# Optimization experiments

Hardware: AMD Instinct MI355X
Metric: run time of the kernel (lower is better)

Reference implementation:

```python
import jax, jax.numpy as jnp
import numpy as np

NEAR, FAR = 0.05, 6.0
STEPSIZE = 0.5
ALPHA_INIT = 1e-6
XYZ_MIN = np.array([-1.0, -1.0, -1.0], np.float32)
XYZ_MAX = np.array([1.0, 1.0, 1.0], np.float32)
WORLD = (160, 160, 160)
VOXEL_SIZE = 2.0 / 160.0  # ((prod span)/num_voxels)^(1/3)
N_SAMPLES = int(np.linalg.norm(np.array(WORLD) + 1) / STEPSIZE) + 1  # 558
ACT_SHIFT = float(np.log(1.0 / (1.0 - ALPHA_INIT) - 1.0))


def setup_inputs() -> dict:
    key = jax.random.key(0)
    k1, k2, k3, k4, k5, k6, k7 = jax.random.split(key, 7)
    rays_o = (jax.random.uniform(k1, (8192, 3), jnp.float32) - 0.5) * 1.2  # inside bbox
    rd = jax.random.normal(k2, (8192, 3), jnp.float32)
    rays_d = rd / jnp.linalg.norm(rd, axis=-1, keepdims=True)
    jitter = jax.random.uniform(k3, (8192, 1), jnp.float32)
    em_modes = jax.random.randint(k4, (8192,), 0, 2, jnp.int32)
    density = jax.random.normal(k5, (1, 160, 160, 160), jnp.float32) * 0.1
    off_color = jax.random.normal(k6, (3, 160, 160, 160), jnp.float32) * 0.1
    emo_color = jax.random.normal(k7, (3, 160, 160, 160), jnp.float32) * 0.1
    return {"rays_o": rays_o, "rays_d": rays_d, "jitter": jitter, "em_modes": em_modes,
            "density": density, "off_color": off_color, "emo_color": emo_color}


def grid_sampler(pts, grid):
    """Trilinear interp, align_corners=True, zero padding. grid [C,Nx,Ny,Nz], pts [...,3] -> [...,C]."""
    C = grid.shape[0]
    sizes = np.array(grid.shape[1:], np.int32)
    lead = pts.shape[:-1]
    t = (pts.reshape(-1, 3) - XYZ_MIN) / (XYZ_MAX - XYZ_MIN)
    idx = t * (jnp.asarray(sizes, pts.dtype) - 1)  # voxel-space coords
    i0 = jnp.floor(idx).astype(jnp.int32)
    f = idx - i0.astype(pts.dtype)
    out = jnp.zeros((i0.shape[0], C), grid.dtype)
    for corner in range(8):
        off = np.array([(corner >> 2) & 1, (corner >> 1) & 1, corner & 1], np.int32)
        ci = i0 + off  # [N,3]
        w = jnp.prod(jnp.where(off[None, :] == 1, f, 1.0 - f), axis=-1)  # [N]
        valid = jnp.all((ci >= 0) & (ci < sizes[None, :]), axis=-1)
        cc = jnp.clip(ci, 0, sizes[None, :] - 1)
        vals = grid[:, cc[:, 0], cc[:, 1], cc[:, 2]].T  # [N,C]
        out = out + (w * valid)[:, None] * vals
    return out.reshape(*lead, C)


def sample_ray(rays_o, rays_d, jitter):
    vec = jnp.where(rays_d == 0, 1e-6, rays_d)
    rate_a = (XYZ_MAX - rays_o) / vec
    rate_b = (XYZ_MIN - rays_o) / vec
    t_min = jnp.clip(jnp.minimum(rate_a, rate_b).max(-1), NEAR, FAR)
    t_max = jnp.clip(jnp.maximum(rate_a, rate_b).min(-1), NEAR, FAR)
    mask_out = t_max <= t_min  # [R]
    rng = jnp.arange(N_SAMPLES, dtype=rays_o.dtype)[None, :] + jitter  # [R,S]
    step = STEPSIZE * VOXEL_SIZE * rng
    interpx = t_min[:, None] + step / jnp.linalg.norm(rays_d, axis=-1, keepdims=True)
    rays_pts = rays_o[:, None, :] + rays_d[:, None, :] * interpx[..., None]  # [R,S,3]
    mask_out = mask_out[:, None] | ((rays_pts < XYZ_MIN) | (rays_pts > XYZ_MAX)).any(-1)
    return rays_pts, mask_out


def reference(rays_o, rays_d, jitter, em_modes, density, off_color, emo_color):
    rays_pts, mask_out = sample_ray(rays_o, rays_d, jitter)
    dens = grid_sampler(rays_pts, density)[..., 0]  # [R,S]
    alpha_all = 1.0 - jnp.exp(-jax.nn.softplus(dens + ACT_SHIFT) * STEPSIZE)
    alpha = jnp.where(mask_out, 0.0, alpha_all)
    p = jnp.clip(1.0 - alpha, 1e-10, None)
    alphainv_cum = jnp.concatenate([jnp.ones_like(p[..., :1]), jnp.cumprod(p, -1)], -1)  # [R,S+1]
    weights = alpha * alphainv_cum[..., :-1]
    on_mask = (em_modes == 1)[:, None, None]
    emo = jax.nn.sigmoid(grid_sampler(rays_pts, emo_color))
    off = jax.nn.sigmoid(grid_sampler(rays_pts, off_color))
    rgb = jnp.where(on_mask, emo, 0.0) + off  # [R,S,3]
    rgb_marched = (weights[..., None] * rgb).sum(-2)  # [R,3]
    return (alphainv_cum, weights, alphainv_cum[..., -1:], rgb, rgb_marched)
```

## Files before the change

kernel.cpp:

```cpp
#include <hip/hip_runtime.h>
#include <math.h>


namespace {
constexpr int   kR   = 8192;
constexpr int   kS   = 558;
constexpr int   kG   = 160;
constexpr int   kG3  = kG * kG * kG;
constexpr float kNear = 0.05f;
constexpr float kFar  = 6.0f;
constexpr float kStepWorld = 0.5f * (2.0f / 160.0f);
constexpr float kActShift = -13.815509557963774f;
constexpr float kLog2e = 1.4426950408889634f;
constexpr int   kBX = 80, kBY = 80, kBZ = 40;
constexpr int   kNB = kBX * kBY * kBZ;
constexpr int   kGridWords = kNB * 16;
}

typedef unsigned int nuint4 __attribute__((ext_vector_type(4)));
typedef float        nfloat2 __attribute__((ext_vector_type(2)));
typedef float        nfloat4 __attribute__((ext_vector_type(4)));

__device__ __forceinline__ float fexp(float x) {
  return __builtin_amdgcn_exp2f(x * kLog2e);
}
__device__ __forceinline__ float sigmoidf_(float x) {
  return __builtin_amdgcn_rcpf(1.0f + fexp(-x));
}

__global__ __launch_bounds__(256) void repack_grids(
    const float* __restrict__ density,
    const float* __restrict__ off_c,
    const float* __restrict__ emo_c,
    unsigned* __restrict__ gridA,
    unsigned* __restrict__ gridB)
{
  const int t   = blockIdx.x * blockDim.x + threadIdx.x;
  const int bid = t >> 2;
  const int q   = t & 3;
  if (bid >= kNB) return;
  const int bz = bid % kBZ;
  const int u  = bid / kBZ;
  const int by = u % kBY;
  const int bx = u / kBY;
  const int x  = bx * 2 + (q >> 1);
  const int y  = by * 2 + (q & 1);
  const int z0 = bz * 4;
  const int vbase = (x * kG + y) * kG + z0;

  const nfloat4 d  = __builtin_nontemporal_load((const nfloat4*)(density + vbase));
  const nfloat4 f0 = __builtin_nontemporal_load((const nfloat4*)(off_c + vbase));
  const nfloat4 f1 = __builtin_nontemporal_load((const nfloat4*)(off_c + vbase + kG3));
  const nfloat4 f2 = __builtin_nontemporal_load((const nfloat4*)(off_c + vbase + 2 * kG3));
  const nfloat4 e0 = __builtin_nontemporal_load((const nfloat4*)(emo_c + vbase));
  const nfloat4 e1 = __builtin_nontemporal_load((const nfloat4*)(emo_c + vbase + kG3));
  const nfloat4 e2 = __builtin_nontemporal_load((const nfloat4*)(emo_c + vbase + 2 * kG3));

  nuint4 va, vb;
  #pragma unroll
  for (int lz = 0; lz < 4; ++lz) {
    int qa = __builtin_amdgcn_cvt_pk_fp8_f32(d[lz],  f0[lz], 0,  false);
    qa     = __builtin_amdgcn_cvt_pk_fp8_f32(f1[lz], f2[lz], qa, true);
    int qb = __builtin_amdgcn_cvt_pk_fp8_f32(e0[lz], e1[lz], 0,  false);
    qb     = __builtin_amdgcn_cvt_pk_fp8_f32(e2[lz], 0.0f,   qb, true);
    va[lz] = (unsigned)qa;
    vb[lz] = (unsigned)qb;
  }
  const size_t woff = (size_t)bid * 16 + q * 4;
  __builtin_nontemporal_store(va, (nuint4*)(gridA + woff));
  __builtin_nontemporal_store(vb, (nuint4*)(gridB + woff));
}

__device__ __forceinline__ int brick_widx(int gx, int gy, int gz) {
  return (((gx >> 1) * kBY + (gy >> 1)) * kBZ + (gz >> 2)) * 16 +
         ((gx & 1) * 2 + (gy & 1)) * 4 + (gz & 3);
}

__global__ __launch_bounds__(256) void dvgo_fwd(
    const float* __restrict__ rays_o,
    const float* __restrict__ rays_d,
    const float* __restrict__ jitter,
    const int*   __restrict__ em_modes,
    const unsigned* __restrict__ gridA,
    const unsigned* __restrict__ gridB,
    float* __restrict__ out)
{
  const int tid  = blockIdx.x * blockDim.x + threadIdx.x;
  const int ray  = tid >> 6;
  const int lane = tid & 63;
  if (ray >= kR) return;

  const float ox = rays_o[ray * 3 + 0];
  const float oy = rays_o[ray * 3 + 1];
  const float oz = rays_o[ray * 3 + 2];
  const float dx = rays_d[ray * 3 + 0];
  const float dy = rays_d[ray * 3 + 1];
  const float dz = rays_d[ray * 3 + 2];
  const float jit = jitter[ray];
  const bool  on  = (em_modes[ray] == 1);

  const float vx = (dx == 0.0f) ? 1e-6f : dx;
  const float vy = (dy == 0.0f) ? 1e-6f : dy;
  const float vz = (dz == 0.0f) ? 1e-6f : dz;
  const float ivx = __builtin_amdgcn_rcpf(vx);
  const float ivy = __builtin_amdgcn_rcpf(vy);
  const float ivz = __builtin_amdgcn_rcpf(vz);
  const float rax = ( 1.0f - ox) * ivx, rbx = (-1.0f - ox) * ivx;
  const float ray_a = ( 1.0f - oy) * ivy, rby = (-1.0f - oy) * ivy;
  const float raz = ( 1.0f - oz) * ivz, rbz = (-1.0f - oz) * ivz;
  float tmin = fmaxf(fmaxf(fminf(rax, rbx), fminf(ray_a, rby)), fminf(raz, rbz));
  float tmax = fminf(fminf(fmaxf(rax, rbx), fmaxf(ray_a, rby)), fmaxf(raz, rbz));
  tmin = fminf(fmaxf(tmin, kNear), kFar);
  tmax = fminf(fmaxf(tmax, kNear), kFar);
  const bool  ray_out = (tmax <= tmin);
  const float stepc = kStepWorld *
      __builtin_amdgcn_rsqf(dx * dx + dy * dy + dz * dz);

  float* out_ainv = out;
  float* out_w    = out + (size_t)kR * (kS + 1);
  float* out_last = out_w + (size_t)kR * kS;
  float* out_rgb  = out_last + kR;
  float* out_rm   = out_rgb + (size_t)kR * kS * 3;

  if (lane == 0)
    __builtin_nontemporal_store(1.0f, out_ainv + (size_t)ray * (kS + 1));

  const float c_base = on ? 1.0f : 0.5f;

  float carry = 1.0f;
  float accr = 0.0f, accg = 0.0f, accb = 0.0f;
  bool dead = false;

  #pragma unroll 1
  for (int chunk = 0; chunk < (kS + 63) / 64; ++chunk) {
    const int  s      = chunk * 64 + lane;
    const bool active = (s < kS);

    if (!dead) {
      const float t  = tmin + stepc * ((float)s + jit);
      const float px = fmaf(dx, t, ox);
      const float py = fmaf(dy, t, oy);
      const float pz = fmaf(dz, t, oz);
      const bool inb = (px >= -1.0f) & (px <= 1.0f) &
                       (py >= -1.0f) & (py <= 1.0f) &
                       (pz >= -1.0f) & (pz <= 1.0f);
      const bool masked = ray_out || !inb;

      const float fx = (px + 1.0f) * 0.5f * (float)(kG - 1);
      const float fy = (py + 1.0f) * 0.5f * (float)(kG - 1);
      const float fz = (pz + 1.0f) * 0.5f * (float)(kG - 1);
      const int ix = (int)floorf(fx);
      const int iy = (int)floorf(fy);
      const int iz = (int)floorf(fz);

      const bool reach = active &&
          (ix >= -1) && (ix <= kG - 1) &&
          (iy >= -1) && (iy <= kG - 1) &&
          (iz >= -1) && (iz <= kG - 1);
      if (__ballot(reach) == 0ull) {
        dead = true;
      } else {
        const float wx = fx - (float)ix;
        const float wy = fy - (float)iy;
        const float wz = fz - (float)iz;
        const float x0 = 1.0f - wx, y0 = 1.0f - wy, z0 = 1.0f - wz;
        const float wxy00 = x0 * y0, wxy01 = x0 * wy;
        const float wxy10 = wx * y0, wxy11 = wx * wy;
        float w8[8];
        w8[0] = wxy00 * z0; w8[1] = wxy00 * wz;
        w8[2] = wxy01 * z0; w8[3] = wxy01 * wz;
        w8[4] = wxy10 * z0; w8[5] = wxy10 * wz;
        w8[6] = wxy11 * z0; w8[7] = wxy11 * wz;

        float dsum = 0.0f;
        float o0 = 0.0f, o1 = 0.0f, o2 = 0.0f;
        float e0 = 0.0f, e1 = 0.0f, e2 = 0.0f;

        const bool interior = active &&
            (ix >= 0) && (ix < kG - 1) &&
            (iy >= 0) && (iy < kG - 1) &&
            (iz >= 0) && (iz < kG - 1);

        if (interior) {
          const int bx = ix >> 1, lx = ix & 1;
          const int by = iy >> 1, ly = iy & 1;
          const int bz = iz >> 2, lz = iz & 3;
          const int bz1 = (iz + 1) >> 2, lz1 = (iz + 1) & 3;
          const int r00 = (bx * kBY + by) * kBZ;
          const int r10 = r00 + lx * (kBY * kBZ);
          const int r01 = r00 + ly * kBZ;
          const int r11 = r10 + ly * kBZ;
          const int sx0 = (lx) * 2,      sx1 = (lx ^ 1) * 2;
          const int sy0 = ly,            sy1 = ly ^ 1;
          int widx[8];
          widx[0] = (r00 + bz ) * 16 + (sx0 + sy0) * 4 + lz;
          widx[1] = (r00 + bz1) * 16 + (sx0 + sy0) * 4 + lz1;
          widx[2] = (r01 + bz ) * 16 + (sx0 + sy1) * 4 + lz;
          widx[3] = (r01 + bz1) * 16 + (sx0 + sy1) * 4 + lz1;
          widx[4] = (r10 + bz ) * 16 + (sx1 + sy0) * 4 + lz;
          widx[5] = (r10 + bz1) * 16 + (sx1 + sy0) * 4 + lz1;
          widx[6] = (r11 + bz ) * 16 + (sx1 + sy1) * 4 + lz;
          widx[7] = (r11 + bz1) * 16 + (sx1 + sy1) * 4 + lz1;

          unsigned ua[8];
          #pragma unroll
          for (int c = 0; c < 8; ++c) ua[c] = gridA[widx[c]];
          if (on) {
            unsigned ub[8];
            #pragma unroll
            for (int c = 0; c < 8; ++c) ub[c] = gridB[widx[c]];
            #pragma unroll
            for (int c = 0; c < 8; ++c) {
              const float w = w8[c];
              dsum = fmaf(w, __builtin_amdgcn_cvt_f32_fp8((int)ua[c], 0), dsum);
              o0   = fmaf(w, __builtin_amdgcn_cvt_f32_fp8((int)ua[c], 1), o0);
              o1   = fmaf(w, __builtin_amdgcn_cvt_f32_fp8((int)ua[c], 2), o1);
              o2   = fmaf(w, __builtin_amdgcn_cvt_f32_fp8((int)ua[c], 3), o2);
              e0   = fmaf(w, __builtin_amdgcn_cvt_f32_fp8((int)ub[c], 0), e0);
              e1   = fmaf(w, __builtin_amdgcn_cvt_f32_fp8((int)ub[c], 1), e1);
              e2   = fmaf(w, __builtin_amdgcn_cvt_f32_fp8((int)ub[c], 2), e2);
            }
          } else {
            #pragma unroll
            for (int c = 0; c < 8; ++c) {
              const float w = w8[c];
              dsum = fmaf(w, __builtin_amdgcn_cvt_f32_fp8((int)ua[c], 0), dsum);
              o0   = fmaf(w, __builtin_amdgcn_cvt_f32_fp8((int)ua[c], 1), o0);
              o1   = fmaf(w, __builtin_amdgcn_cvt_f32_fp8((int)ua[c], 2), o1);
              o2   = fmaf(w, __builtin_amdgcn_cvt_f32_fp8((int)ua[c], 3), o2);
            }
          }
        } else if (reach) {
          #pragma unroll
          for (int c = 0; c < 8; ++c) {
            const int cx = ix + ((c >> 2) & 1);
            const int cy = iy + ((c >> 1) & 1);
            const int cz = iz + (c & 1);
            const bool valid = ((unsigned)cx < (unsigned)kG) &
                               ((unsigned)cy < (unsigned)kG) &
                               ((unsigned)cz < (unsigned)kG);
            const float wv = valid ? w8[c] : 0.0f;
            const int gx = min(max(cx, 0), kG - 1);
            const int gy = min(max(cy, 0), kG - 1);
            const int gz = min(max(cz, 0), kG - 1);
            const int wi = brick_widx(gx, gy, gz);
            const unsigned qa = gridA[wi];
            dsum = fmaf(wv, __builtin_amdgcn_cvt_f32_fp8((int)qa, 0), dsum);
            o0   = fmaf(wv, __builtin_amdgcn_cvt_f32_fp8((int)qa, 1), o0);
            o1   = fmaf(wv, __builtin_amdgcn_cvt_f32_fp8((int)qa, 2), o1);
            o2   = fmaf(wv, __builtin_amdgcn_cvt_f32_fp8((int)qa, 3), o2);
            if (on) {
              const unsigned qb = gridB[wi];
              e0 = fmaf(wv, __builtin_amdgcn_cvt_f32_fp8((int)qb, 0), e0);
              e1 = fmaf(wv, __builtin_amdgcn_cvt_f32_fp8((int)qb, 1), e1);
              e2 = fmaf(wv, __builtin_amdgcn_cvt_f32_fp8((int)qb, 2), e2);
            }
          }
        }

        float p = 1.0f;
        if (active && !masked) {
          const float ex = fexp(dsum + kActShift);
          p = fmaxf(__builtin_amdgcn_rsqf(1.0f + ex), 1e-10f);
        }
        const float alpha = 1.0f - p;

        float incl = p;
        #pragma unroll
        for (int o = 1; o < 64; o <<= 1) {
          const float n = __shfl_up(incl, o, 64);
          if (lane >= o) incl *= n;
        }
        float excl = __shfl_up(incl, 1, 64);
        if (lane == 0) excl = 1.0f;
        const float ainv_prev = carry * excl;
        const float ainv_next = carry * incl;
        const float wgt = alpha * ainv_prev;
        carry *= __shfl(incl, 63, 64);

        float rr = sigmoidf_(o0);
        float gg = sigmoidf_(o1);
        float bb = sigmoidf_(o2);
        if (on) {
          rr += sigmoidf_(e0);
          gg += sigmoidf_(e1);
          bb += sigmoidf_(e2);
        }

        if (active) {
          __builtin_nontemporal_store(ainv_next,
              out_ainv + (size_t)ray * (kS + 1) + s + 1);
          __builtin_nontemporal_store(wgt, out_w + (size_t)ray * kS + s);
          const size_t rb = ((size_t)ray * kS + s) * 3;
          nfloat2 rg;
          rg.x = rr; rg.y = gg;
          __builtin_nontemporal_store(rg, (nfloat2*)(out_rgb + rb));
          __builtin_nontemporal_store(bb, out_rgb + rb + 2);
          accr = fmaf(wgt, rr, accr);
          accg = fmaf(wgt, gg, accg);
          accb = fmaf(wgt, bb, accb);
        }
        continue;
      }
    }

    if (active) {
      __builtin_nontemporal_store(carry,
          out_ainv + (size_t)ray * (kS + 1) + s + 1);
      __builtin_nontemporal_store(0.0f, out_w + (size_t)ray * kS + s);
      const size_t rb = ((size_t)ray * kS + s) * 3;
      nfloat2 cb;
      cb.x = c_base; cb.y = c_base;
      __builtin_nontemporal_store(cb, (nfloat2*)(out_rgb + rb));
      __builtin_nontemporal_store(c_base, out_rgb + rb + 2);
    }
  }

  #pragma unroll
  for (int o = 32; o > 0; o >>= 1) {
    accr += __shfl_xor(accr, o, 64);
    accg += __shfl_xor(accg, o, 64);
    accb += __shfl_xor(accb, o, 64);
  }
  if (lane == 0) {
    out_last[ray] = carry;
    out_rm[(size_t)ray * 3 + 0] = accr;
    out_rm[(size_t)ray * 3 + 1] = accg;
    out_rm[(size_t)ray * 3 + 2] = accb;
  }
}

extern "C" void kernel_launch(void* const* d_in, const int* in_sizes, int n_in,
                              void* d_out, int out_size, void* d_ws, size_t ws_size,
                              hipStream_t stream) {
  const float* rays_o  = (const float*)d_in[0];
  const float* rays_d  = (const float*)d_in[1];
  const float* jitter  = (const float*)d_in[2];
  const int*   em      = (const int*)d_in[3];
  const float* density = (const float*)d_in[4];
  const float* off_c   = (const float*)d_in[5];
  const float* emo_c   = (const float*)d_in[6];
  float* out = (float*)d_out;

  unsigned* gridA = (unsigned*)d_ws;
  unsigned* gridB = gridA + kGridWords;
  (void)ws_size;

  hipLaunchKernelGGL(repack_grids, dim3((kNB * 4 + 255) / 256), dim3(256), 0,
                     stream, density, off_c, emo_c, gridA, gridB);

  const int threads = 256;
  const int blocks  = (kR * 64) / threads;
  hipLaunchKernelGGL(dvgo_fwd, dim3(blocks), dim3(threads), 0, stream,
                     rays_o, rays_d, jitter, em, gridA, gridB, out);
}
```

Baseline: 225.5 us.

## Software-pipeline grid gathers one chunk ahead and unify boundary sampling path

Restructures the per-ray chunk loop so the eight trilinear corner gathers for the next 64-sample chunk are issued before the current chunk's scan, sigmoid and store work, hiding global memory latency behind compute. Interior and boundary samples now share one branch-free path that clamps addresses and zeroes weights for invalid corners. It also replaces size_t index math with 32-bit ints. In exchange, the loaded words and geometry are kept live across iterations, which raises register pressure, and the position math is computed twice per chunk.

Measured after the change: 220.2 us. -2.4%, faster.

```diff
diff --git a/kernel.cpp b/kernel.cpp
--- a/kernel.cpp
+++ b/kernel.cpp
@@ -5,6 +5,7 @@
 namespace {
 constexpr int   kR   = 8192;
 constexpr int   kS   = 558;
+constexpr int   kNC  = (kS + 63) / 64;
 constexpr int   kG   = 160;
 constexpr int   kG3  = kG * kG * kG;
 constexpr float kNear = 0.05f;
@@ -15,6 +16,8 @@
 constexpr int   kBX = 80, kBY = 80, kBZ = 40;
 constexpr int   kNB = kBX * kBY * kBZ;
 constexpr int   kGridWords = kNB * 16;
+constexpr int   kXS = kBY * kBZ * 16;
+constexpr int   kYS = kBZ * 16;
 }
 
 typedef unsigned int nuint4 __attribute__((ext_vector_type(4)));
@@ -71,11 +74,6 @@
   __builtin_nontemporal_store(vb, (nuint4*)(gridB + woff));
 }
 
-__device__ __forceinline__ int brick_widx(int gx, int gy, int gz) {
-  return (((gx >> 1) * kBY + (gy >> 1)) * kBZ + (gz >> 2)) * 16 +
-         ((gx & 1) * 2 + (gy & 1)) * 4 + (gz & 3);
-}
-
 __global__ __launch_bounds__(256) void dvgo_fwd(
     const float* __restrict__ rays_o,
     const float* __restrict__ rays_d,
@@ -117,203 +115,218 @@
       __builtin_amdgcn_rsqf(dx * dx + dy * dy + dz * dz);
 
   float* out_ainv = out;
-  float* out_w    = out + (size_t)kR * (kS + 1);
-  float* out_last = out_w + (size_t)kR * kS;
+  float* out_w    = out + kR * (kS + 1);
+  float* out_last = out_w + kR * kS;
   float* out_rgb  = out_last + kR;
-  float* out_rm   = out_rgb + (size_t)kR * kS * 3;
+  float* out_rm   = out_rgb + kR * kS * 3;
+
+  const int base_ainv = ray * (kS + 1);
+  const int base_w    = ray * kS;
 
   if (lane == 0)
-    __builtin_nontemporal_store(1.0f, out_ainv + (size_t)ray * (kS + 1));
+    __builtin_nontemporal_store(1.0f, out_ainv + base_ainv);
 
   const float c_base = on ? 1.0f : 0.5f;
+
+  auto geom_addr = [&](int chunk, int wi[8]) -> unsigned long long {
+    const int   s  = chunk * 64 + lane;
+    const bool  ac = (s < kS);
+    const float t  = tmin + stepc * ((float)s + jit);
+    const float px = fmaf(dx, t, ox);
+    const float py = fmaf(dy, t, oy);
+    const float pz = fmaf(dz, t, oz);
+    const float fx = (px + 1.0f) * 0.5f * (float)(kG - 1);
+    const float fy = (py + 1.0f) * 0.5f * (float)(kG - 1);
+    const float fz = (pz + 1.0f) * 0.5f * (float)(kG - 1);
+    const int ix = (int)floorf(fx);
+    const int iy = (int)floorf(fy);
+    const int iz = (int)floorf(fz);
+    const bool reach = ac &&
+        (ix >= -1) && (ix <= kG - 1) &&
+        (iy >= -1) && (iy <= kG - 1) &&
+        (iz >= -1) && (iz <= kG - 1);
+    const int gx0 = min(max(ix, 0), kG - 1),     gx1 = min(max(ix + 1, 0), kG - 1);
+    const int gy0 = min(max(iy, 0), kG - 1),     gy1 = min(max(iy + 1, 0), kG - 1);
+    const int gz0 = min(max(iz, 0), kG - 1),     gz1 = min(max(iz + 1, 0), kG - 1);
+    const int X0 = (gx0 >> 1) * kXS + (gx0 & 1) * 8;
+    const int X1 = (gx1 >> 1) * kXS + (gx1 & 1) * 8;
+    const int Y0 = (gy0 >> 1) * kYS + (gy0 & 1) * 4;
+    const int Y1 = (gy1 >> 1) * kYS + (gy1 & 1) * 4;
+    const int Z0 = (gz0 >> 2) * 16 + (gz0 & 3);
+    const int Z1 = (gz1 >> 2) * 16 + (gz1 & 3);
+    wi[0] = X0 + Y0 + Z0; wi[1] = X0 + Y0 + Z1;
+    wi[2] = X0 + Y1 + Z0; wi[3] = X0 + Y1 + Z1;
+    wi[4] = X1 + Y0 + Z0; wi[5] = X1 + Y0 + Z1;
+    wi[6] = X1 + Y1 + Z0; wi[7] = X1 + Y1 + Z1;
+    return __ballot(reach);
+  };
+
+  auto geom_w = [&](int chunk, float w8[8], bool& masked, bool& active) {
+    const int   s  = chunk * 64 + lane;
+    active = (s < kS);
+    const float t  = tmin + stepc * ((float)s + jit);
+    const float px = fmaf(dx, t, ox);
+    const float py = fmaf(dy, t, oy);
+    const float pz = fmaf(dz, t, oz);
+    const bool inb = (px >= -1.0f) & (px <= 1.0f) &
+                     (py >= -1.0f) & (py <= 1.0f) &
+                     (pz >= -1.0f) & (pz <= 1.0f);
+    masked = ray_out || !inb;
+    const float fx = (px + 1.0f) * 0.5f * (float)(kG - 1);
+    const float fy = (py + 1.0f) * 0.5f * (float)(kG - 1);
+    const float fz = (pz + 1.0f) * 0.5f * (float)(kG - 1);
+    const int ix = (int)floorf(fx);
+    const int iy = (int)floorf(fy);
+    const int iz = (int)floorf(fz);
+    const float wx = fx - (float)ix;
+    const float wy = fy - (float)iy;
+    const float wz = fz - (float)iz;
+    const float x0 = 1.0f - wx, y0 = 1.0f - wy, z0 = 1.0f - wz;
+    const float wxy00 = x0 * y0, wxy01 = x0 * wy;
+    const float wxy10 = wx * y0, wxy11 = wx * wy;
+    const bool vx0 = ((unsigned)ix       < (unsigned)kG);
+    const bool vx1 = ((unsigned)(ix + 1) < (unsigned)kG);
+    const bool vy0 = ((unsigned)iy       < (unsigned)kG);
+    const bool vy1 = ((unsigned)(iy + 1) < (unsigned)kG);
+    const bool vz0 = ((unsigned)iz       < (unsigned)kG);
+    const bool vz1 = ((unsigned)(iz + 1) < (unsigned)kG);
+    w8[0] = (vx0 & vy0 & vz0) ? wxy00 * z0 : 0.0f;
+    w8[1] = (vx0 & vy0 & vz1) ? wxy00 * wz : 0.0f;
+    w8[2] = (vx0 & vy1 & vz0) ? wxy01 * z0 : 0.0f;
+    w8[3] = (vx0 & vy1 & vz1) ? wxy01 * wz : 0.0f;
+    w8[4] = (vx1 & vy0 & vz0) ? wxy10 * z0 : 0.0f;
+    w8[5] = (vx1 & vy0 & vz1) ? wxy10 * wz : 0.0f;
+    w8[6] = (vx1 & vy1 & vz0) ? wxy11 * z0 : 0.0f;
+    w8[7] = (vx1 & vy1 & vz1) ? wxy11 * wz : 0.0f;
+  };
 
   float carry = 1.0f;
   float accr = 0.0f, accg = 0.0f, accb = 0.0f;
-  bool dead = false;
+
+  unsigned ua[8] = {0, 0, 0, 0, 0, 0, 0, 0};
+  unsigned ub[8] = {0, 0, 0, 0, 0, 0, 0, 0};
+  bool dead_pipe = false;
+  bool cur_dead  = true;
+
+  {
+    int wi[8];
+    const unsigned long long bal = geom_addr(0, wi);
+    if (bal == 0ull) {
+      dead_pipe = true;
+    } else {
+      cur_dead = false;
+      #pragma unroll
+      for (int c = 0; c < 8; ++c) ua[c] = gridA[wi[c]];
+      if (on) {
+        #pragma unroll
+        for (int c = 0; c < 8; ++c) ub[c] = gridB[wi[c]];
+      }
+    }
+  }
 
   #pragma unroll 1
-  for (int chunk = 0; chunk < (kS + 63) / 64; ++chunk) {
-    const int  s      = chunk * 64 + lane;
-    const bool active = (s < kS);
-
-    if (!dead) {
-      const float t  = tmin + stepc * ((float)s + jit);
-      const float px = fmaf(dx, t, ox);
-      const float py = fmaf(dy, t, oy);
-      const float pz = fmaf(dz, t, oz);
-      const bool inb = (px >= -1.0f) & (px <= 1.0f) &
-                       (py >= -1.0f) & (py <= 1.0f) &
-                       (pz >= -1.0f) & (pz <= 1.0f);
-      const bool masked = ray_out || !inb;
-
-      const float fx = (px + 1.0f) * 0.5f * (float)(kG - 1);
-      const float fy = (py + 1.0f) * 0.5f * (float)(kG - 1);
-      const float fz = (pz + 1.0f) * 0.5f * (float)(kG - 1);
-      const int ix = (int)floorf(fx);
-      const int iy = (int)floorf(fy);
-      const int iz = (int)floorf(fz);
-
-      const bool reach = active &&
-          (ix >= -1) && (ix <= kG - 1) &&
-          (iy >= -1) && (iy <= kG - 1) &&
-          (iz >= -1) && (iz <= kG - 1);
-      if (__ballot(reach) == 0ull) {
-        dead = true;
+  for (int chunk = 0; chunk < kNC; ++chunk) {
+    const int  s       = chunk * 64 + lane;
+    const bool active0 = (s < kS);
+
+    float dsum = 0.0f;
+    float o0 = 0.0f, o1 = 0.0f, o2 = 0.0f;
+    float e0 = 0.0f, e1 = 0.0f, e2 = 0.0f;
+    bool masked = true, active = active0;
+
+    if (!cur_dead) {
+      float w8[8];
+      geom_w(chunk, w8, masked, active);
+      #pragma unroll
+      for (int c = 0; c < 8; ++c) {
+        const float w = w8[c];
+        dsum = fmaf(w, __builtin_amdgcn_cvt_f32_fp8((int)ua[c], 0), dsum);
+        o0   = fmaf(w, __builtin_amdgcn_cvt_f32_fp8((int)ua[c], 1), o0);
+        o1   = fmaf(w, __builtin_amdgcn_cvt_f32_fp8((int)ua[c], 2), o1);
+        o2   = fmaf(w, __builtin_amdgcn_cvt_f32_fp8((int)ua[c], 3), o2);
+      }
+      if (on) {
+        #pragma unroll
+        for (int c = 0; c < 8; ++c) {
+          const float w = w8[c];
+          e0 = fmaf(w, __builtin_amdgcn_cvt_f32_fp8((int)ub[c], 0), e0);
+          e1 = fmaf(w, __builtin_amdgcn_cvt_f32_fp8((int)ub[c], 1), e1);
+          e2 = fmaf(w, __builtin_amdgcn_cvt_f32_fp8((int)ub[c], 2), e2);
+        }
+      }
+    }
+
+    bool nxt_dead = true;
+    if (!dead_pipe && (chunk + 1) < kNC) {
+      int wi[8];
+      const unsigned long long bal = geom_addr(chunk + 1, wi);
+      if (bal == 0ull) {
+        dead_pipe = true;
       } else {
-        const float wx = fx - (float)ix;
-        const float wy = fy - (float)iy;
-        const float wz = fz - (float)iz;
-        const float x0 = 1.0f - wx, y0 = 1.0f - wy, z0 = 1.0f - wz;
-        const float wxy00 = x0 * y0, wxy01 = x0 * wy;
-        const float wxy10 = wx * y0, wxy11 = wx * wy;
-        float w8[8];
-        w8[0] = wxy00 * z0; w8[1] = wxy00 * wz;
-        w8[2] = wxy01 * z0; w8[3] = wxy01 * wz;
-        w8[4] = wxy10 * z0; w8[5] = wxy10 * wz;
-        w8[6] = wxy11 * z0; w8[7] = wxy11 * wz;
-
-        float dsum = 0.0f;
-        float o0 = 0.0f, o1 = 0.0f, o2 = 0.0f;
-        float e0 = 0.0f, e1 = 0.0f, e2 = 0.0f;
-
-        const bool interior = active &&
-            (ix >= 0) && (ix < kG - 1) &&
-            (iy >= 0) && (iy < kG - 1) &&
-            (iz >= 0) && (iz < kG - 1);
-
-        if (interior) {
-          const int bx = ix >> 1, lx = ix & 1;
-          const int by = iy >> 1, ly = iy & 1;
-          const int bz = iz >> 2, lz = iz & 3;
-          const int bz1 = (iz + 1) >> 2, lz1 = (iz + 1) & 3;
-          const int r00 = (bx * kBY + by) * kBZ;
-          const int r10 = r00 + lx * (kBY * kBZ);
-          const int r01 = r00 + ly * kBZ;
-          const int r11 = r10 + ly * kBZ;
-          const int sx0 = (lx) * 2,      sx1 = (lx ^ 1) * 2;
-          const int sy0 = ly,            sy1 = ly ^ 1;
-          int widx[8];
-          widx[0] = (r00 + bz ) * 16 + (sx0 + sy0) * 4 + lz;
-          widx[1] = (r00 + bz1) * 16 + (sx0 + sy0) * 4 + lz1;
-          widx[2] = (r01 + bz ) * 16 + (sx0 + sy1) * 4 + lz;
-          widx[3] = (r01 + bz1) * 16 + (sx0 + sy1) * 4 + lz1;
-          widx[4] = (r10 + bz ) * 16 + (sx1 + sy0) * 4 + lz;
-          widx[5] = (r10 + bz1) * 16 + (sx1 + sy0) * 4 + lz1;
-          widx[6] = (r11 + bz ) * 16 + (sx1 + sy1) * 4 + lz;
-          widx[7] = (r11 + bz1) * 16 + (sx1 + sy1) * 4 + lz1;
-
-          unsigned ua[8];
+        nxt_dead = false;
+        #pragma unroll
+        for (int c = 0; c < 8; ++c) ua[c] = gridA[wi[c]];
+        if (on) {
           #pragma unroll
-          for (int c = 0; c < 8; ++c) ua[c] = gridA[widx[c]];
-          if (on) {
-            unsigned ub[8];
-            #pragma unroll
-            for (int c = 0; c < 8; ++c) ub[c] = gridB[widx[c]];
-            #pragma unroll
-            for (int c = 0; c < 8; ++c) {
-              const float w = w8[c];
-              dsum = fmaf(w, __builtin_amdgcn_cvt_f32_fp8((int)ua[c], 0), dsum);
-              o0   = fmaf(w, __builtin_amdgcn_cvt_f32_fp8((int)ua[c], 1), o0);
-              o1   = fmaf(w, __builtin_amdgcn_cvt_f32_fp8((int)ua[c], 2), o1);
-              o2   = fmaf(w, __builtin_amdgcn_cvt_f32_fp8((int)ua[c], 3), o2);
-              e0   = fmaf(w, __builtin_amdgcn_cvt_f32_fp8((int)ub[c], 0), e0);
-              e1   = fmaf(w, __builtin_amdgcn_cvt_f32_fp8((int)ub[c], 1), e1);
-              e2   = fmaf(w, __builtin_amdgcn_cvt_f32_fp8((int)ub[c], 2), e2);
-            }
-          } else {
-            #pragma unroll
-            for (int c = 0; c < 8; ++c) {
-              const float w = w8[c];
-              dsum = fmaf(w, __builtin_amdgcn_cvt_f32_fp8((int)ua[c], 0), dsum);
-              o0   = fmaf(w, __builtin_amdgcn_cvt_f32_fp8((int)ua[c], 1), o0);
-              o1   = fmaf(w, __builtin_amdgcn_cvt_f32_fp8((int)ua[c], 2), o1);
-              o2   = fmaf(w, __builtin_amdgcn_cvt_f32_fp8((int)ua[c], 3), o2);
-            }
-          }
-        } else if (reach) {
-          #pragma unroll
-          for (int c = 0; c < 8; ++c) {
-            const int cx = ix + ((c >> 2) & 1);
-            const int cy = iy + ((c >> 1) & 1);
-            const int cz = iz + (c & 1);
-            const bool valid = ((unsigned)cx < (unsigned)kG) &
-                               ((unsigned)cy < (unsigned)kG) &
-                               ((unsigned)cz < (unsigned)kG);
-            const float wv = valid ? w8[c] : 0.0f;
-            const int gx = min(max(cx, 0), kG - 1);
-            const int gy = min(max(cy, 0), kG - 1);
-            const int gz = min(max(cz, 0), kG - 1);
-            const int wi = brick_widx(gx, gy, gz);
-            const unsigned qa = gridA[wi];
-            dsum = fmaf(wv, __builtin_amdgcn_cvt_f32_fp8((int)qa, 0), dsum);
-            o0   = fmaf(wv, __builtin_amdgcn_cvt_f32_fp8((int)qa, 1), o0);
-            o1   = fmaf(wv, __builtin_amdgcn_cvt_f32_fp8((int)qa, 2), o1);
-            o2   = fmaf(wv, __builtin_amdgcn_cvt_f32_fp8((int)qa, 3), o2);
-            if (on) {
-              const unsigned qb = gridB[wi];
-              e0 = fmaf(wv, __builtin_amdgcn_cvt_f32_fp8((int)qb, 0), e0);
-              e1 = fmaf(wv, __builtin_amdgcn_cvt_f32_fp8((int)qb, 1), e1);
-              e2 = fmaf(wv, __builtin_amdgcn_cvt_f32_fp8((int)qb, 2), e2);
-            }
-          }
+          for (int c = 0; c < 8; ++c) ub[c] = gridB[wi[c]];
         }
-
-        float p = 1.0f;
-        if (active && !masked) {
-          const float ex = fexp(dsum + kActShift);
-          p = fmaxf(__builtin_amdgcn_rsqf(1.0f + ex), 1e-10f);
-        }
-        const float alpha = 1.0f - p;
-
-        float incl = p;
-        #pragma unroll
-        for (int o = 1; o < 64; o <<= 1) {
-          const float n = __shfl_up(incl, o, 64);
-          if (lane >= o) incl *= n;
-        }
-        float excl = __shfl_up(incl, 1, 64);
-        if (lane == 0) excl = 1.0f;
-        const float ainv_prev = carry * excl;
-        const float ainv_next = carry * incl;
-        const float wgt = alpha * ainv_prev;
-        carry *= __shfl(incl, 63, 64);
-
-        float rr = sigmoidf_(o0);
-        float gg = sigmoidf_(o1);
-        float bb = sigmoidf_(o2);
-        if (on) {
-          rr += sigmoidf_(e0);
-          gg += sigmoidf_(e1);
-          bb += sigmoidf_(e2);
-        }
-
-        if (active) {
-          __builtin_nontemporal_store(ainv_next,
-              out_ainv + (size_t)ray * (kS + 1) + s + 1);
-          __builtin_nontemporal_store(wgt, out_w + (size_t)ray * kS + s);
-          const size_t rb = ((size_t)ray * kS + s) * 3;
-          nfloat2 rg;
-          rg.x = rr; rg.y = gg;
-          __builtin_nontemporal_store(rg, (nfloat2*)(out_rgb + rb));
-          __builtin_nontemporal_store(bb, out_rgb + rb + 2);
-          accr = fmaf(wgt, rr, accr);
-          accg = fmaf(wgt, gg, accg);
-          accb = fmaf(wgt, bb, accb);
-        }
-        continue;
       }
     }
 
-    if (active) {
-      __builtin_nontemporal_store(carry,
-          out_ainv + (size_t)ray * (kS + 1) + s + 1);
-      __builtin_nontemporal_store(0.0f, out_w + (size_t)ray * kS + s);
-      const size_t rb = ((size_t)ray * kS + s) * 3;
+    if (!cur_dead) {
+      float p = 1.0f;
+      if (active && !masked) {
+        const float expx = fexp(dsum + kActShift);
+        p = fmaxf(__builtin_amdgcn_rsqf(1.0f + expx), 1e-10f);
+      }
+      const float alpha = 1.0f - p;
+
+      float incl = p;
+      #pragma unroll
+      for (int o = 1; o < 64; o <<= 1) {
+        const float n = __shfl_up(incl, o, 64);
+        if (lane >= o) incl *= n;
+      }
+      float excl = __shfl_up(incl, 1, 64);
+      if (lane == 0) excl = 1.0f;
+
+      const float ainv_prev = carry * excl;
+      const float ainv_next = carry * incl;
+      const float wgt = alpha * ainv_prev;
+      carry *= __shfl(incl, 63, 64);
+
+      float rr = sigmoidf_(o0);
+      float gg = sigmoidf_(o1);
+      float bb = sigmoidf_(o2);
+      if (on) {
+        rr += sigmoidf_(e0);
+        gg += sigmoidf_(e1);
+        bb += sigmoidf_(e2);
+      }
+
+      if (active) {
+        __builtin_nontemporal_store(ainv_next, out_ainv + base_ainv + s + 1);
+        __builtin_nontemporal_store(wgt, out_w + base_w + s);
+        const int rb = (base_w + s) * 3;
+        nfloat2 rg;
+        rg.x = rr; rg.y = gg;
+        __builtin_nontemporal_store(rg, (nfloat2*)(out_rgb + rb));
+        __builtin_nontemporal_store(bb, out_rgb + rb + 2);
+        accr = fmaf(wgt, rr, accr);
+        accg = fmaf(wgt, gg, accg);
+        accb = fmaf(wgt, bb, accb);
+      }
+    } else if (active0) {
+      __builtin_nontemporal_store(carry, out_ainv + base_ainv + s + 1);
+      __builtin_nontemporal_store(0.0f, out_w + base_w + s);
+      const int rb = (base_w + s) * 3;
       nfloat2 cb;
       cb.x = c_base; cb.y = c_base;
       __builtin_nontemporal_store(cb, (nfloat2*)(out_rgb + rb));
       __builtin_nontemporal_store(c_base, out_rgb + rb + 2);
     }
+
+    cur_dead = nxt_dead;
   }
 
   #pragma unroll
@@ -324,9 +337,9 @@
   }
   if (lane == 0) {
     out_last[ray] = carry;
-    out_rm[(size_t)ray * 3 + 0] = accr;
-    out_rm[(size_t)ray * 3 + 1] = accg;
-    out_rm[(size_t)ray * 3 + 2] = accb;
+    out_rm[ray * 3 + 0] = accr;
+    out_rm[ray * 3 + 1] = accg;
+    out_rm[ray * 3 + 2] = accb;
   }
 }
 
```
